# Kernel optimization log

Measured on AMD Instinct MI355X. Metric: run time of the kernel, lower is better.

Reference implementation:

```python
import jax, jax.numpy as jnp
import numpy as np

E = 128    # embedding_size
N = 8192   # total vertices (64 graphs x 128)
CN = 512   # total color slots
G = 64     # number of graphs
TMAX = 32


def _mlp3(x, W, b):
    # 3-layer MLP: Linear-ReLU-Linear-ReLU-Linear. W: [3,E,E], b: [3,E]
    h = jax.nn.relu(x @ W[0].T + b[0])
    h = jax.nn.relu(h @ W[1].T + b[1])
    return h @ W[2].T + b[2]


def _lstm_cell(x, h, c, Wih, Whh, bih, bhh):
    # PyTorch LSTM gate order: i, f, g, o
    gates = x @ Wih.T + h @ Whh.T + (bih + bhh)
    i, f, g, o = jnp.split(gates, 4, axis=-1)
    c2 = jax.nn.sigmoid(f) * c + jax.nn.sigmoid(i) * jnp.tanh(g)
    h2 = jax.nn.sigmoid(o) * jnp.tanh(c2)
    return h2, c2


def setup_inputs() -> dict:
    key = jax.random.key(0)
    ks = jax.random.split(key, 24)
    s = 1.0 / np.sqrt(E)
    f32 = jnp.float32
    inp = {
        "M_vv": jax.random.normal(ks[0], (N, N), f32) * s,
        "M_vc": jax.random.uniform(ks[1], (N, CN), f32) * (1.0 / np.sqrt(CN)),
        "C": jax.random.normal(ks[2], (CN, E), f32),
        "slice_idx": jnp.full((G,), N // G, dtype=jnp.int32),
        "v_emb_w": jax.random.normal(ks[3], (E, 1), f32) * s,
        "v_emb_b": jax.random.normal(ks[4], (E,), f32) * s,
        "mlpC_W": jax.random.normal(ks[5], (3, E, E), f32) * s,
        "mlpC_b": jax.random.normal(ks[6], (3, E), f32) * s,
        "mlpV_W": jax.random.normal(ks[7], (3, E, E), f32) * s,
        "mlpV_b": jax.random.normal(ks[8], (3, E), f32) * s,
        "Wih_v": jax.random.normal(ks[9], (4 * E, 2 * E), f32) * s,
        "Whh_v": jax.random.normal(ks[10], (4 * E, E), f32) * s,
        "bih_v": jax.random.normal(ks[11], (4 * E,), f32) * s,
        "bhh_v": jax.random.normal(ks[12], (4 * E,), f32) * s,
        "Wih_c": jax.random.normal(ks[13], (4 * E, E), f32) * s,
        "Whh_c": jax.random.normal(ks[14], (4 * E, E), f32) * s,
        "bih_c": jax.random.normal(ks[15], (4 * E,), f32) * s,
        "bhh_c": jax.random.normal(ks[16], (4 * E,), f32) * s,
        "vote_W1": jax.random.normal(ks[17], (E, E), f32) * s,
        "vote_b1": jax.random.normal(ks[18], (E,), f32) * s,
        "vote_W2": jax.random.normal(ks[19], (E, E), f32) * s,
        "vote_b2": jax.random.normal(ks[20], (E,), f32) * s,
        "vote_W3": jax.random.normal(ks[21], (1, E), f32) * s,
        "vote_b3": jax.random.normal(ks[22], (1,), f32) * s,
    }
    return inp


def reference(M_vv, M_vc, C, slice_idx, v_emb_w, v_emb_b, mlpC_W, mlpC_b,
              mlpV_W, mlpV_b, Wih_v, Whh_v, bih_v, bhh_v, Wih_c, Whh_c,
              bih_c, bhh_c, vote_W1, vote_b1, vote_W2, vote_b2, vote_W3, vote_b3):
    n = M_vv.shape[0]
    g = slice_idx.shape[0]
    # V = v_emb(ones(1)) broadcast to all vertices: [N, E]
    v0 = v_emb_w[:, 0] + v_emb_b
    V = jnp.broadcast_to(v0, (n, E))
    # Original torch loop never reassigns V, so both LSTM inputs are
    # loop-invariant; compute them once (identical math, no recompute).
    x_v = jnp.concatenate([M_vv @ V, M_vc @ _mlp3(C, mlpC_W, mlpC_b)], axis=1)  # [N, 2E]
    x_c = M_vc.T @ _mlp3(V, mlpV_W, mlpV_b)                                      # [CN, E]

    def step(carry, _):
        hv, cv, hc, cc = carry
        hv, cv = _lstm_cell(x_v, hv, cv, Wih_v, Whh_v, bih_v, bhh_v)
        hc, cc = _lstm_cell(x_c, hc, cc, Wih_c, Whh_c, bih_c, bhh_c)
        return (hv, cv, hc, cc), None

    init = (V, jnp.zeros_like(V), C, jnp.zeros_like(C))
    (hv, cv, hc, cc), _ = jax.lax.scan(step, init, None, length=TMAX)

    # vote MLP on final vertex hidden state -> [N, 1]
    h = jax.nn.relu(hv @ vote_W1.T + vote_b1)
    h = jax.nn.relu(h @ vote_W2.T + vote_b2)
    v_vote = (h @ vote_W3.T + vote_b3)[:, 0]  # [N]

    # per-graph mean then sigmoid (torch: split + mean + sigmoid + vstack)
    seg = jnp.repeat(jnp.arange(g), slice_idx, total_repeat_length=n)
    sums = jax.ops.segment_sum(v_vote, seg, num_segments=g)
    ret = jax.nn.sigmoid(sums / slice_idx.astype(sums.dtype))
    return (ret, V[None], C)
```

## Files before the change

kernel.cpp:

```cpp
#include <hip/hip_runtime.h>
#include <hip/hip_bf16.h>
#include <stdint.h>


typedef __bf16 bf16x8 __attribute__((ext_vector_type(8)));
typedef float f32x4 __attribute__((ext_vector_type(4)));

#define EDIM 128
#define NVERT 8192
#define CNUM 512
#define NG 64
#define TSTEPS 32
#define ROWS 16

#define WS_CNT 0u
#define WS_V0 32768u
#define WS_W1 33280u
#define WS_BV 35328u
#define WS_ACC 37376u
#define WS_V0BF 37632u
#define WS_MLPC3T 38912u

__device__ __forceinline__ float bf2f(unsigned short s) {
  return __uint_as_float(((unsigned)s) << 16);
}
__device__ __forceinline__ unsigned short f2bf(float f) {
  unsigned u = __float_as_uint(f);
  u += 0x7fffu + ((u >> 16) & 1u);
  return (unsigned short)(u >> 16);
}
__device__ __forceinline__ float sigm(float x) {
  return __builtin_amdgcn_rcpf(1.f + __expf(-x));
}
__device__ __forceinline__ float tanh_f(float x) {
  return 1.f - 2.f * __builtin_amdgcn_rcpf(1.f + __expf(2.f * x));
}
__device__ __forceinline__ f32x4 mfma16(bf16x8 a, bf16x8 b, f32x4 c) {
  return __builtin_amdgcn_mfma_f32_16x16x32_bf16(a, b, c, 0, 0, 0);
}
__device__ __forceinline__ bf16x8 ld8(const float* p) {
  float4 a = *(const float4*)p;
  float4 b = *(const float4*)(p + 4);
  bf16x8 r;
  r[0] = (__bf16)a.x; r[1] = (__bf16)a.y; r[2] = (__bf16)a.z; r[3] = (__bf16)a.w;
  r[4] = (__bf16)b.x; r[5] = (__bf16)b.y; r[6] = (__bf16)b.z; r[7] = (__bf16)b.w;
  return r;
}

__global__ __launch_bounds__(128) void k_setup(
    const float* __restrict__ C, const float* __restrict__ W,
    const float* __restrict__ B, const float* __restrict__ vw,
    const float* __restrict__ vb, const float* __restrict__ Wih,
    const float* __restrict__ bih, const float* __restrict__ bhh,
    float* __restrict__ ws, float* __restrict__ Cout) {
  __shared__ float xb[2][EDIM];
  const int t = threadIdx.x;

  if (blockIdx.x == CNUM) {
    float* v0 = (float*)((char*)ws + WS_V0);
    float* w1 = (float*)((char*)ws + WS_W1);
    float* bvp = (float*)((char*)ws + WS_BV);
    float* acc = (float*)((char*)ws + WS_ACC);
    unsigned short* v0bf = (unsigned short*)((char*)ws + WS_V0BF);
    unsigned int* cnt = (unsigned int*)((char*)ws + WS_CNT);
    float v = vw[t] + vb[t];
    xb[0][t] = v;
    v0[t] = v;
    v0bf[t] = f2bf(v);
    if (t < NG) acc[t] = 0.f;
    if (t == 0) *cnt = 0u;
    __syncthreads();
#pragma unroll
    for (int gi = 0; gi < 4; gi++) {
      const int col = gi * EDIM + t;
      const float4* wr = (const float4*)(Wih + (size_t)col * 256);
      float s = 0.f;
#pragma unroll
      for (int kc = 0; kc < 32; kc++) {
        float4 q = wr[kc];
        const float* xi = xb[0] + kc * 4;
        s += q.x * xi[0] + q.y * xi[1] + q.z * xi[2] + q.w * xi[3];
      }
      w1[col] = s;
      bvp[col] = bih[col] + bhh[col];
    }
    return;
  }

  unsigned short* out_t = (unsigned short*)((char*)ws + WS_MLPC3T);
  const int c = blockIdx.x, e = t;
  float cval = C[c * EDIM + e];
  xb[0][e] = cval;
  Cout[c * EDIM + e] = cval;
  __syncthreads();
#pragma unroll
  for (int l = 0; l < 3; l++) {
    const float4* wrow = (const float4*)(W + ((size_t)l * EDIM + e) * EDIM);
    const float* xin = xb[l & 1];
    float s = B[l * EDIM + e];
#pragma unroll
    for (int kc = 0; kc < EDIM / 4; kc++) {
      float4 q = wrow[kc];
      const float* xi = xin + kc * 4;
      s += q.x * xi[0] + q.y * xi[1] + q.z * xi[2] + q.w * xi[3];
    }
    if (l < 2) {
      s = fmaxf(s, 0.f);
      __syncthreads();
      xb[(l + 1) & 1][e] = s;
      __syncthreads();
    } else {
      out_t[(size_t)e * CNUM + c] = f2bf(s);
    }
  }
}

__global__ __launch_bounds__(512, 4) void k_main(
    const float* __restrict__ Mvv, const float* __restrict__ Mvc,
    const float* __restrict__ Wih, const float* __restrict__ Whh,
    const float* __restrict__ W1, const float* __restrict__ b1,
    const float* __restrict__ W2, const float* __restrict__ b2,
    const float* __restrict__ W3, const float* __restrict__ b3,
    const int* __restrict__ slice, float* __restrict__ ws,
    float* __restrict__ out) {
  const int r0 = blockIdx.x * ROWS;
  const int t = threadIdx.x;
  const int w = t >> 6;
  const int lane = t & 63;
  const int quad = lane >> 4;
  const int l15 = lane & 15;
  const int nc0 = w * 16;

  __shared__ unsigned short Avc[ROWS][CNUM + 8];
  __shared__ unsigned short Tt[ROWS][EDIM + 8];
  __shared__ unsigned short hv2[2][ROWS][EDIM + 8];
  __shared__ float votes[ROWS];
  __shared__ float rs_s[ROWS];
  __shared__ unsigned int last_s;

  const float* w1v = (const float*)((const char*)ws + WS_W1);
  const float* bvv = (const float*)((const char*)ws + WS_BV);
  float* accg = (float*)((char*)ws + WS_ACC);
  unsigned int* cnt = (unsigned int*)((char*)ws + WS_CNT);
  const unsigned short* v0bf = (const unsigned short*)((const char*)ws + WS_V0BF);
  const unsigned short* m3t = (const unsigned short*)((const char*)ws + WS_MLPC3T);

  {
    const int row = t >> 5, c0 = t & 31;
    const float4* g = (const float4*)(Mvc + (size_t)(r0 + row) * CNUM);
    float4 av[4];
#pragma unroll
    for (int it = 0; it < 4; it++) av[it] = g[it * 32 + c0];

    const float4* mp = (const float4*)(Mvv + (size_t)(r0 + row) * NVERT) + c0;
    float s = 0.f;
#pragma unroll 1
    for (int ch = 0; ch < 4; ch++) {
      float4 q[16];
#pragma unroll
      for (int j = 0; j < 16; j++) q[j] = mp[ch * 512 + j * 32];
#pragma unroll
      for (int j = 0; j < 16; j++) s += q[j].x + q[j].y + q[j].z + q[j].w;
    }
    s += __shfl_down(s, 16, 32);
    s += __shfl_down(s, 8, 32);
    s += __shfl_down(s, 4, 32);
    s += __shfl_down(s, 2, 32);
    s += __shfl_down(s, 1, 32);
    if (c0 == 0) rs_s[row] = s;

#pragma unroll
    for (int it = 0; it < 4; it++) {
      int c4 = it * 32 + c0;
      ushort4 h;
      h.x = f2bf(av[it].x); h.y = f2bf(av[it].y);
      h.z = f2bf(av[it].z); h.w = f2bf(av[it].w);
      *(ushort4*)&Avc[row][c4 * 4] = h;
    }
  }
  {
    const float4* v04 = (const float4*)((const char*)ws + WS_V0);
    float4* V4 = (float4*)(out + NG);
    int vr = t >> 5, vc = t & 31;
    V4[(size_t)(r0 + vr) * 32 + vc] = v04[vc];
  }
  for (int i = t; i < ROWS * EDIM; i += 512) hv2[0][i >> 7][i & 127] = v0bf[i & 127];
  __syncthreads();

  {
    f32x4 acc;
    acc[0] = 0.f; acc[1] = 0.f; acc[2] = 0.f; acc[3] = 0.f;
#pragma unroll
    for (int kc = 0; kc < 16; kc++) {
      bf16x8 a0 = *(const bf16x8*)&Avc[l15][kc * 32 + quad * 8];
      bf16x8 b0 = *(const bf16x8*)&m3t[(size_t)(nc0 + l15) * CNUM + kc * 32 + quad * 8];
      acc = mfma16(a0, b0, acc);
    }
#pragma unroll
    for (int r = 0; r < 4; r++)
      Tt[quad * 4 + r][nc0 + l15] = f2bf(acc[r]);
  }
  __syncthreads();

  f32x4 xg[4];
  {
    float rsv[4];
#pragma unroll
    for (int r = 0; r < 4; r++) rsv[r] = rs_s[quad * 4 + r];
#pragma unroll
    for (int gi = 0; gi < 4; gi++) {
      const int col = gi * 128 + nc0 + l15;
      const float w1c = w1v[col], bvc = bvv[col];
#pragma unroll
      for (int r = 0; r < 4; r++) xg[gi][r] = fmaf(rsv[r], w1c, bvc);
    }
#pragma unroll
    for (int kc = 0; kc < 4; kc++) {
      bf16x8 a0 = *(const bf16x8*)&Tt[l15][kc * 32 + quad * 8];
#pragma unroll
      for (int gi = 0; gi < 4; gi++) {
        const int gcol = gi * 128 + nc0 + l15;
        bf16x8 bfr = ld8(&Wih[(size_t)gcol * 256 + 128 + kc * 32 + quad * 8]);
        xg[gi] = mfma16(a0, bfr, xg[gi]);
      }
    }
  }

  bf16x8 Bh[4][4];
#pragma unroll
  for (int gi = 0; gi < 4; gi++) {
    const int gcol = gi * 128 + nc0 + l15;
#pragma unroll
    for (int kc = 0; kc < 4; kc++)
      Bh[gi][kc] = ld8(&Whh[(size_t)gcol * EDIM + kc * 32 + quad * 8]);
  }

  f32x4 cv;
  cv[0] = 0.f; cv[1] = 0.f; cv[2] = 0.f; cv[3] = 0.f;

  int p = 0;
#pragma unroll 1
  for (int step = 0; step < TSTEPS; step++) {
    bf16x8 A[4];
#pragma unroll
    for (int kc = 0; kc < 4; kc++)
      A[kc] = *(const bf16x8*)&hv2[p][l15][kc * 32 + quad * 8];
    f32x4 gI = xg[0], gF = xg[1], gG = xg[2], gO = xg[3];
#pragma unroll
    for (int kc = 0; kc < 4; kc++) {
      gI = mfma16(A[kc], Bh[0][kc], gI);
      gF = mfma16(A[kc], Bh[1][kc], gF);
      gG = mfma16(A[kc], Bh[2][kc], gG);
      gO = mfma16(A[kc], Bh[3][kc], gO);
    }
#pragma unroll
    for (int r = 0; r < 4; r++) {
      float ig = sigm(gI[r]), fg = sigm(gF[r]);
      float gg = tanh_f(gG[r]), og = sigm(gO[r]);
      float c2 = fmaf(fg, cv[r], ig * gg);
      cv[r] = c2;
      hv2[p ^ 1][quad * 4 + r][nc0 + l15] = f2bf(og * tanh_f(c2));
    }
    p ^= 1;
    __syncthreads();
  }

  for (int layer = 0; layer < 2; layer++) {
    const float* Wg = layer ? W2 : W1;
    const float* bg = layer ? b2 : b1;
    bf16x8 A[4];
#pragma unroll
    for (int kc = 0; kc < 4; kc++)
      A[kc] = *(const bf16x8*)&hv2[0][l15][kc * 32 + quad * 8];
    f32x4 acc;
    {
      float bb = bg[nc0 + l15];
      acc[0] = bb; acc[1] = bb; acc[2] = bb; acc[3] = bb;
    }
#pragma unroll
    for (int kc = 0; kc < 4; kc++) {
      bf16x8 bfr = ld8(&Wg[(size_t)(nc0 + l15) * EDIM + kc * 32 + quad * 8]);
      acc = mfma16(A[kc], bfr, acc);
    }
    __syncthreads();
#pragma unroll
    for (int r = 0; r < 4; r++)
      hv2[0][quad * 4 + r][nc0 + l15] = f2bf(fmaxf(acc[r], 0.f));
    __syncthreads();
  }

  {
    if (t < 16 * ROWS) {
      const int row = t >> 4, seg = t & 15;
      float part = 0.f;
#pragma unroll
      for (int j = 0; j < 8; j++) {
        const int k = seg * 8 + j;
        part += bf2f(hv2[0][row][k]) * W3[k];
      }
      part += __shfl_down(part, 8, 16);
      part += __shfl_down(part, 4, 16);
      part += __shfl_down(part, 2, 16);
      part += __shfl_down(part, 1, 16);
      if (seg == 0) votes[row] = part + b3[0];
    }
    __syncthreads();
    if (t < 64) {
      float v = (t < ROWS) ? votes[t] : 0.f;
#pragma unroll
      for (int off = 32; off > 0; off >>= 1) v += __shfl_down(v, off, 64);
      if (t == 0) atomicAdd(&accg[blockIdx.x >> 3], v);
    }
  }

  if (t == 0) {
    __threadfence();
    last_s = atomicAdd(cnt, 1u);
  }
  __syncthreads();
  if (last_s == 8 * NG - 1) {
    __threadfence();
    if (t < NG) {
      float v = __hip_atomic_load(&accg[t], __ATOMIC_ACQUIRE,
                                  __HIP_MEMORY_SCOPE_AGENT);
      float m = v / (float)slice[t];
      out[t] = 1.f / (1.f + __expf(-m));
    }
  }
}

extern "C" void kernel_launch(void* const* d_in, const int* in_sizes, int n_in,
                              void* d_out, int out_size, void* d_ws, size_t ws_size,
                              hipStream_t stream) {
  const float* M_vv = (const float*)d_in[0];
  const float* M_vc = (const float*)d_in[1];
  const float* C = (const float*)d_in[2];
  const int* slice = (const int*)d_in[3];
  const float* vw = (const float*)d_in[4];
  const float* vb = (const float*)d_in[5];
  const float* mW = (const float*)d_in[6];
  const float* mB = (const float*)d_in[7];
  const float* Wih = (const float*)d_in[10];
  const float* Whh = (const float*)d_in[11];
  const float* bih = (const float*)d_in[12];
  const float* bhh = (const float*)d_in[13];
  const float* W1 = (const float*)d_in[18];
  const float* b1 = (const float*)d_in[19];
  const float* W2 = (const float*)d_in[20];
  const float* b2 = (const float*)d_in[21];
  const float* W3 = (const float*)d_in[22];
  const float* b3 = (const float*)d_in[23];
  float* ws = (float*)d_ws;
  float* out = (float*)d_out;

  k_setup<<<CNUM + 1, 128, 0, stream>>>(C, mW, mB, vw, vb, Wih, bih, bhh, ws,
                                        out + NG + (size_t)NVERT * EDIM);
  k_main<<<NVERT / ROWS, 512, 0, stream>>>(M_vv, M_vc, Wih, Whh, W1, b1, W2,
                                           b2, W3, b3, slice, ws, out);
}
```

Measured before the change: 504.4 us.

## Split M_vv row-sum into a separate high-occupancy streaming kernel

Moves the full-row reduction of the large M_vv matrix, and the write of the V output, out of the main LSTM kernel into a new kernel. The new kernel uses 2048 blocks of 256 threads, one wavefront per row, to stream M_vv. The main kernel then reads the precomputed row sums from a new workspace slot, and the other workspace offsets shift to make room. This is meant to raise memory-level parallelism for the bandwidth-bound read and to slim the LSTM kernel. The cost is an extra launch and lost overlap between the streaming read and the LSTM compute.

```diff
diff --git a/kernel.cpp b/kernel.cpp
--- a/kernel.cpp
+++ b/kernel.cpp
@@ -14,11 +14,12 @@
 #define ROWS 16
 
 #define WS_CNT 0u
-#define WS_V0 32768u
-#define WS_W1 33280u
-#define WS_BV 35328u
-#define WS_ACC 37376u
-#define WS_V0BF 37632u
+#define WS_RS 1024u
+#define WS_V0 33792u
+#define WS_W1 34304u
+#define WS_BV 36352u
+#define WS_ACC 38400u
+#define WS_V0BF 38656u
 #define WS_MLPC3T 38912u
 
 __device__ __forceinline__ float bf2f(unsigned short s) {
@@ -115,9 +116,37 @@
   }
 }
 
-__global__ __launch_bounds__(512, 4) void k_main(
-    const float* __restrict__ Mvv, const float* __restrict__ Mvc,
-    const float* __restrict__ Wih, const float* __restrict__ Whh,
+__global__ __launch_bounds__(256, 8) void k_rowsum(
+    const float* __restrict__ Mvv, const float* __restrict__ ws_c,
+    float* __restrict__ ws, float* __restrict__ out) {
+  const int t = threadIdx.x;
+  const int lane = t & 63;
+  const int row = blockIdx.x * 4 + (t >> 6);
+  const float4* rp = (const float4*)(Mvv + (size_t)row * NVERT);
+
+  f32x4 acc;
+  acc[0] = 0.f; acc[1] = 0.f; acc[2] = 0.f; acc[3] = 0.f;
+#pragma unroll
+  for (int j = 0; j < 32; j++) {
+    float4 q = rp[j * 64 + lane];
+    acc[0] += q.x; acc[1] += q.y; acc[2] += q.z; acc[3] += q.w;
+  }
+  float s = (acc[0] + acc[1]) + (acc[2] + acc[3]);
+#pragma unroll
+  for (int off = 32; off > 0; off >>= 1) s += __shfl_down(s, off, 64);
+  if (lane == 0) ((float*)((char*)ws + WS_RS))[row] = s;
+
+  if (t < 128) {
+    const float4* v04 = (const float4*)((const char*)ws_c + WS_V0);
+    float4* V4 = (float4*)(out + NG);
+    int vr = t >> 5, vc = t & 31;
+    V4[(size_t)(blockIdx.x * 4 + vr) * 32 + vc] = v04[vc];
+  }
+}
+
+__global__ __launch_bounds__(512, 4) void k_lstm(
+    const float* __restrict__ Mvc, const float* __restrict__ Wih,
+    const float* __restrict__ Whh,
     const float* __restrict__ W1, const float* __restrict__ b1,
     const float* __restrict__ W2, const float* __restrict__ b2,
     const float* __restrict__ W3, const float* __restrict__ b3,
@@ -140,35 +169,20 @@
 
   const float* w1v = (const float*)((const char*)ws + WS_W1);
   const float* bvv = (const float*)((const char*)ws + WS_BV);
+  const float* rsg = (const float*)((const char*)ws + WS_RS);
   float* accg = (float*)((char*)ws + WS_ACC);
   unsigned int* cnt = (unsigned int*)((char*)ws + WS_CNT);
   const unsigned short* v0bf = (const unsigned short*)((const char*)ws + WS_V0BF);
   const unsigned short* m3t = (const unsigned short*)((const char*)ws + WS_MLPC3T);
 
+  if (t < ROWS) rs_s[t] = rsg[r0 + t];
+
   {
     const int row = t >> 5, c0 = t & 31;
     const float4* g = (const float4*)(Mvc + (size_t)(r0 + row) * CNUM);
     float4 av[4];
 #pragma unroll
     for (int it = 0; it < 4; it++) av[it] = g[it * 32 + c0];
-
-    const float4* mp = (const float4*)(Mvv + (size_t)(r0 + row) * NVERT) + c0;
-    float s = 0.f;
-#pragma unroll 1
-    for (int ch = 0; ch < 4; ch++) {
-      float4 q[16];
-#pragma unroll
-      for (int j = 0; j < 16; j++) q[j] = mp[ch * 512 + j * 32];
-#pragma unroll
-      for (int j = 0; j < 16; j++) s += q[j].x + q[j].y + q[j].z + q[j].w;
-    }
-    s += __shfl_down(s, 16, 32);
-    s += __shfl_down(s, 8, 32);
-    s += __shfl_down(s, 4, 32);
-    s += __shfl_down(s, 2, 32);
-    s += __shfl_down(s, 1, 32);
-    if (c0 == 0) rs_s[row] = s;
-
 #pragma unroll
     for (int it = 0; it < 4; it++) {
       int c4 = it * 32 + c0;
@@ -177,12 +191,6 @@
       h.z = f2bf(av[it].z); h.w = f2bf(av[it].w);
       *(ushort4*)&Avc[row][c4 * 4] = h;
     }
-  }
-  {
-    const float4* v04 = (const float4*)((const char*)ws + WS_V0);
-    float4* V4 = (float4*)(out + NG);
-    int vr = t >> 5, vc = t & 31;
-    V4[(size_t)(r0 + vr) * 32 + vc] = v04[vc];
   }
   for (int i = t; i < ROWS * EDIM; i += 512) hv2[0][i >> 7][i & 127] = v0bf[i & 127];
   __syncthreads();
@@ -355,6 +363,7 @@
 
   k_setup<<<CNUM + 1, 128, 0, stream>>>(C, mW, mB, vw, vb, Wih, bih, bhh, ws,
                                         out + NG + (size_t)NVERT * EDIM);
-  k_main<<<NVERT / ROWS, 512, 0, stream>>>(M_vv, M_vc, Wih, Whh, W1, b1, W2,
-                                           b2, W3, b3, slice, ws, out);
-}
+  k_rowsum<<<NVERT / 4, 256, 0, stream>>>(M_vv, ws, ws, out);
+  k_lstm<<<NVERT / ROWS, 512, 0, stream>>>(M_vc, Wih, Whh, W1, b1, W2, b2, W3,
+                                           b3, slice, ws, out);
+}
```

Result: slower. 524.2 us (+3.9%).
